# Kernel tuning notes

Measured on AMD Instinct MI355X. Metric: run time of the kernel, lower is better.

The kernel has to match this reference:

```python
import jax, jax.numpy as jnp
import numpy as np

B, C, D, T = 8, 512, 256, 2048
EPS = 1e-5


def setup_inputs() -> dict:
    key = jax.random.key(0)
    ks = jax.random.split(key, 9)
    s_c = 1.0 / np.sqrt(C)
    s_d = 1.0 / np.sqrt(D)
    return {
        "inpt": jax.random.normal(ks[0], (B, C, T), dtype=jnp.float32),
        "theta_w": jax.random.uniform(ks[1], (D, C), jnp.float32, -s_c, s_c),
        "theta_b": jax.random.uniform(ks[2], (D,), jnp.float32, -s_c, s_c),
        "phi_w": jax.random.uniform(ks[3], (D, C), jnp.float32, -s_c, s_c),
        "phi_b": jax.random.uniform(ks[4], (D,), jnp.float32, -s_c, s_c),
        "g_w": jax.random.uniform(ks[5], (D, C), jnp.float32, -s_c, s_c),
        "g_b": jax.random.uniform(ks[6], (D,), jnp.float32, -s_c, s_c),
        "ht_w": jax.random.uniform(ks[7], (C, D), jnp.float32, -s_d, s_d),
        "ht_b": jax.random.uniform(ks[8], (C,), jnp.float32, -s_d, s_d),
        "bn_gamma": jnp.ones((C,), dtype=jnp.float32),
        "bn_beta": jnp.zeros((C,), dtype=jnp.float32),
    }


def reference(inpt, theta_w, theta_b, phi_w, phi_b, g_w, g_b, ht_w, ht_b, bn_gamma, bn_beta):
    # 1x1 convs are just channel-mixing matmuls: (B,C,T) -> (B,D,T)
    theta = jnp.einsum('dc,bct->bdt', theta_w, inpt) + theta_b[None, :, None]
    phi = jnp.einsum('dc,bct->bdt', phi_w, inpt) + phi_b[None, :, None]
    g = jnp.einsum('dc,bct->bdt', g_w, inpt) + g_b[None, :, None]
    # w[b,t,s] = sum_d theta[b,d,t] * phi[b,d,s]; softmax over s (phi time)
    w = jnp.einsum('bdt,bds->bts', theta, phi)
    w = jax.nn.softmax(w, axis=-1)
    # torch.matmul(g, w): out[b,d,s] = sum_t g[b,d,t] * w[b,t,s]
    attn = jnp.einsum('bdt,bts->bds', g, w)
    # ht 1x1 conv back to C channels
    h = jnp.einsum('cd,bdt->bct', ht_w, attn) + ht_b[None, :, None]
    # BatchNorm1d in training mode: batch stats over (B, T) per channel
    mean = jnp.mean(h, axis=(0, 2), keepdims=True)
    var = jnp.var(h, axis=(0, 2), keepdims=True)  # biased variance
    h_norm = (h - mean) * jax.lax.rsqrt(var + EPS)
    bn = bn_gamma[None, :, None] * h_norm + bn_beta[None, :, None]
    return inpt + bn
```

## Files before the change

kernel.cpp:

```cpp
#include <hip/hip_runtime.h>
#include <hip/hip_bf16.h>
#include <math.h>

#define Bx 8
#define Cx 512
#define Dx 256
#define Tx 2048
#define EPSx 1e-5f

typedef _Float16 h16;
typedef __attribute__((ext_vector_type(8))) _Float16 h16x8;
typedef __attribute__((ext_vector_type(8))) short s16x8;
typedef __attribute__((ext_vector_type(4))) float f32x4;

typedef __attribute__((address_space(3))) unsigned int lds_u32;
typedef __attribute__((address_space(1))) const unsigned int glb_u32;

__device__ __forceinline__ void cp16(void* ldsp, const void* g) {
    __builtin_amdgcn_global_load_lds((glb_u32*)g, (lds_u32*)ldsp, 16, 0, 0);
}

template<int MODE, bool BF>
__global__ __launch_bounds__(256, 4)
void gemm_mf(const h16* __restrict__ A, long aBatch, int lda,
             const h16* __restrict__ B, long bBatch, int ldb,
             void* __restrict__ C, long cBatch, int ldc,
             float* __restrict__ Cp, float* __restrict__ Z,
             int M, int N, int K,
             const float* __restrict__ biasM, const float* __restrict__ biasN) {
    __shared__ h16 As[128 * 64];
    __shared__ h16 Bs[128 * 64];
    const int tid  = threadIdx.x;
    const int lane = tid & 63, wid = tid >> 6;
    const int wm = (wid & 1) * 64, wn = (wid >> 1) * 64;
    const int lm = lane & 15, quad = lane >> 4;
    const int m0 = blockIdx.y * 128, n0 = blockIdx.x * 128;
    const int b = blockIdx.z;
    const h16* Ab = A + (size_t)b * aBatch + (size_t)m0 * lda;
    const h16* Bb = B + (size_t)b * bBatch + (size_t)n0 * ldb;

    const int srow  = tid >> 3;
    const int sclog = (tid & 7) ^ (srow & 7);
    char* ldsA = (char*)As + (tid & ~63) * 16;
    char* ldsB = (char*)Bs + (tid & ~63) * 16;

    f32x4 acc[4][4] = {};

    for (int k0 = 0; k0 < K; k0 += 64) {
        __syncthreads();
#pragma unroll
        for (int i = 0; i < 4; i++) {
            int r = srow + 32 * i;
            cp16(ldsA + i * 4096, Ab + (size_t)r * lda + k0 + sclog * 8);
        }
#pragma unroll
        for (int i = 0; i < 4; i++) {
            int r = srow + 32 * i;
            cp16(ldsB + i * 4096, Bb + (size_t)r * ldb + k0 + sclog * 8);
        }
        __syncthreads();
#pragma unroll
        for (int ks = 0; ks < 2; ks++) {
            s16x8 af[4], bf4[4];
#pragma unroll
            for (int i = 0; i < 4; i++) {
                int row = wm + 16 * i + lm;
                int st = (ks * 4 + quad) ^ (lm & 7);
                af[i] = *(const s16x8*)(As + row * 64 + st * 8);
            }
#pragma unroll
            for (int j = 0; j < 4; j++) {
                int row = wn + 16 * j + lm;
                int st = (ks * 4 + quad) ^ (lm & 7);
                bf4[j] = *(const s16x8*)(Bs + row * 64 + st * 8);
            }
#pragma unroll
            for (int i = 0; i < 4; i++)
#pragma unroll
                for (int j = 0; j < 4; j++) {
                    if constexpr (BF)
                        acc[i][j] = __builtin_amdgcn_mfma_f32_16x16x32_bf16(
                            af[i], bf4[j], acc[i][j], 0, 0, 0);
                    else
                        acc[i][j] = __builtin_amdgcn_mfma_f32_16x16x32_f16(
                            __builtin_bit_cast(h16x8, af[i]),
                            __builtin_bit_cast(h16x8, bf4[j]), acc[i][j], 0, 0, 0);
                }
        }
    }

    if constexpr (MODE == 0) {
        h16* Cb = (h16*)C + (size_t)b * cBatch;
#pragma unroll
        for (int i = 0; i < 4; i++)
#pragma unroll
            for (int j = 0; j < 4; j++) {
                int row = m0 + wm + 16 * i + quad * 4;
                int col = n0 + wn + 16 * j + lm;
                float bN = biasN ? biasN[col] : 0.0f;
#pragma unroll
                for (int r = 0; r < 4; r++) {
                    float v = acc[i][j][r] + bN;
                    if (biasM) v += biasM[row + r];
                    Cb[(size_t)(row + r) * ldc + col] = (h16)v;
                }
            }
    } else if constexpr (MODE == 1) {
        __hip_bfloat16* Cb = (__hip_bfloat16*)C + (size_t)b * cBatch;
#pragma unroll
        for (int j = 0; j < 4; j++) {
            int col = n0 + wn + 16 * j + lm;
            float iz = 1.0f / Z[(size_t)b * N + col];
#pragma unroll
            for (int i = 0; i < 4; i++) {
                int row = m0 + wm + 16 * i + quad * 4;
#pragma unroll
                for (int r = 0; r < 4; r++)
                    Cb[(size_t)(row + r) * ldc + col] =
                        __float2bfloat16(acc[i][j][r] * iz);
            }
        }
    } else if constexpr (MODE == 2) {
        __syncthreads();
        float* Zl = (float*)As;
        if (tid < 128) Zl[tid] = 0.0f;
        __syncthreads();
        __hip_bfloat16* Cb = (__hip_bfloat16*)C + (size_t)b * cBatch;
#pragma unroll
        for (int j = 0; j < 4; j++) {
            int cl = wn + 16 * j + lm;
            int col = n0 + cl;
            float zp = 0.0f;
#pragma unroll
            for (int i = 0; i < 4; i++) {
                int row = m0 + wm + 16 * i + quad * 4;
#pragma unroll
                for (int r = 0; r < 4; r++) {
                    float e = __expf(acc[i][j][r]);
                    zp += e;
                    Cb[(size_t)(row + r) * ldc + col] = __float2bfloat16(e);
                }
            }
            atomicAdd(&Zl[cl], zp);
        }
        __syncthreads();
        if (tid < 128) atomicAdd(&Z[(size_t)b * N + n0 + tid], Zl[tid]);
    } else {
        __syncthreads();
        float* Sl = (float*)As;
        float* Sq = Sl + 128;
        if (tid < 256) Sl[tid] = 0.0f;
        __syncthreads();
        h16* Cb = (h16*)C + (size_t)b * cBatch;
#pragma unroll
        for (int j = 0; j < 4; j++) {
            int cl = wn + 16 * j + lm;
            int col = n0 + cl;
            float bN = biasN[col];
            float s = 0.0f, q = 0.0f;
#pragma unroll
            for (int i = 0; i < 4; i++) {
                int row = m0 + wm + 16 * i + quad * 4;
#pragma unroll
                for (int r = 0; r < 4; r++) {
                    float v = acc[i][j][r] + bN;
                    s += v;
                    q = fmaf(v, v, q);
                    Cb[(size_t)(row + r) * ldc + col] = (h16)v;
                }
            }
            atomicAdd(&Sl[cl], s);
            atomicAdd(&Sq[cl], q);
        }
        __syncthreads();
        if (tid < 128) {
            atomicAdd(&Cp[n0 + tid], Sl[tid]);
            atomicAdd(&Z[n0 + tid], Sq[tid]);
        }
    }
}

__global__ __launch_bounds__(256)
void conv_x(const float* __restrict__ inpt, h16* __restrict__ xT) {
    __shared__ float lds[64][68];
    const int b = blockIdx.z;
    const int t0 = blockIdx.x * 64, c0 = blockIdx.y * 64;
    const int tid = threadIdx.x, q = tid >> 4, k = tid & 15;
    const float* ib = inpt + (size_t)b * Cx * Tx;
#pragma unroll
    for (int i = 0; i < 4; i++) {
        int c = q + 16 * i;
        float4 v = *(const float4*)(ib + (size_t)(c0 + c) * Tx + t0 + 4 * k);
        *(float4*)&lds[c][4 * k] = v;
    }
    __syncthreads();
    h16* xb = xT + (size_t)b * Tx * Cx;
#pragma unroll
    for (int i = 0; i < 4; i++) {
        int t = q + 16 * i;
        h16 o[4];
#pragma unroll
        for (int j = 0; j < 4; j++) o[j] = (h16)lds[4 * k + j][t];
        *(uint2*)(xb + (size_t)(t0 + t) * Cx + c0 + 4 * k) = *(uint2*)o;
    }
}

__global__ __launch_bounds__(256)
void conv_w(const float* __restrict__ w0, const float* __restrict__ w1,
            const float* __restrict__ w2, const float* __restrict__ w3,
            const float* __restrict__ tb, const float* __restrict__ pb,
            const float* __restrict__ gb,
            h16* __restrict__ dst, float* __restrict__ bias3,
            float* __restrict__ Z, float* __restrict__ psum,
            float* __restrict__ pssq) {
    int bx = blockIdx.x;
    int tid = threadIdx.x;
    if (bx == 577) {
        psum[tid] = 0.0f; psum[tid + 256] = 0.0f;
        pssq[tid] = 0.0f; pssq[tid + 256] = 0.0f;
        return;
    }
    if (bx >= 513) { Z[(bx - 513) * 256 + tid] = 0.0f; return; }
    if (bx == 512) {
        bias3[tid] = tb[tid];
        bias3[tid + 256] = pb[tid];
        bias3[tid + 512] = gb[tid];
        return;
    }
    int idx4 = bx * 256 + tid;
    int arr = idx4 >> 15, local4 = idx4 & 32767;
    const float* srcs[4] = {w0, w1, w2, w3};
    float4 v = ((const float4*)srcs[arr])[local4];
    h16 o[4] = {(h16)v.x, (h16)v.y, (h16)v.z, (h16)v.w};
    *(uint2*)(dst + (size_t)arr * 131072 + (size_t)local4 * 4) = *(uint2*)o;
}

__global__ __launch_bounds__(256)
void bn_final(const float* __restrict__ psum, const float* __restrict__ pssq,
              float* __restrict__ mean, float* __restrict__ rsig) {
    int c = blockIdx.x * 256 + threadIdx.x;
    const float invN = 1.0f / (float)(Bx * Tx);
    float mu = psum[c] * invN;
    float var = pssq[c] * invN - mu * mu;
    mean[c] = mu;
    rsig[c] = rsqrtf(var + EPSx);
}

__global__ __launch_bounds__(256)
void bn_apply_T(const float* __restrict__ inpt, const h16* __restrict__ hT,
                const float* __restrict__ mean, const float* __restrict__ rsig,
                const float* __restrict__ gamma, const float* __restrict__ beta,
                float* __restrict__ out) {
    __shared__ float lds[64][68];
    const int b = blockIdx.z, t0 = blockIdx.x * 64, c0 = blockIdx.y * 64;
    const int tid = threadIdx.x, q = tid >> 4, k = tid & 15;
    const h16* hb = hT + (size_t)b * Tx * Cx;
#pragma unroll
    for (int i = 0; i < 4; i++) {
        int t = q + 16 * i;
        uint2 raw = *(const uint2*)(hb + (size_t)(t0 + t) * Cx + c0 + 4 * k);
        const h16* hp = (const h16*)&raw;
        float4 v = make_float4((float)hp[0], (float)hp[1], (float)hp[2], (float)hp[3]);
        *(float4*)&lds[t][4 * k] = v;
    }
    __syncthreads();
    const float* ib = inpt + (size_t)b * Cx * Tx;
    float* ob = out + (size_t)b * Cx * Tx;
#pragma unroll
    for (int i = 0; i < 4; i++) {
        int c = q + 16 * i;
        int cg = c0 + c;
        float mu = mean[cg], rv = rsig[cg], ga = gamma[cg], be = beta[cg];
        float4 x = *(const float4*)(ib + (size_t)cg * Tx + t0 + 4 * k);
        float4 o;
        o.x = x.x + ga * (lds[4 * k + 0][c] - mu) * rv + be;
        o.y = x.y + ga * (lds[4 * k + 1][c] - mu) * rv + be;
        o.z = x.z + ga * (lds[4 * k + 2][c] - mu) * rv + be;
        o.w = x.w + ga * (lds[4 * k + 3][c] - mu) * rv + be;
        *(float4*)(ob + (size_t)cg * Tx + t0 + 4 * k) = o;
    }
}

extern "C" void kernel_launch(void* const* d_in, const int* in_sizes, int n_in,
                              void* d_out, int out_size, void* d_ws, size_t ws_size,
                              hipStream_t stream) {
    const float* inpt    = (const float*)d_in[0];
    const float* theta_w = (const float*)d_in[1];
    const float* theta_b = (const float*)d_in[2];
    const float* phi_w   = (const float*)d_in[3];
    const float* phi_b   = (const float*)d_in[4];
    const float* g_w     = (const float*)d_in[5];
    const float* g_b     = (const float*)d_in[6];
    const float* ht_w    = (const float*)d_in[7];
    const float* ht_b    = (const float*)d_in[8];
    const float* gamma   = (const float*)d_in[9];
    const float* beta    = (const float*)d_in[10];

    char* ws = (char*)d_ws;
    h16*   xT    = (h16*)(ws + 0);
    h16*   w4    = (h16*)(ws + 16777216);
    h16*   wHt   = w4 + 393216;
    float* bias3 = (float*)(ws + 17825792);
    float* Z     = (float*)(ws + 17828864);
    float* psum  = (float*)(ws + 17894400);
    float* pssq  = (float*)(ws + 17896448);
    float* mu    = (float*)(ws + 17898496);
    float* rs    = (float*)(ws + 17900544);
    h16*   thpg  = (h16*)(ws + 17902592);
    h16*   gh    = (h16*)(ws + 43068416);
    h16*   LT    = (h16*)(ws + 59845632);
    h16*   hT    = xT;

    const long sX  = (long)Tx * Cx;
    const long sTP = (long)Tx * 768;
    const long sGH = (long)Cx * Tx;
    const long sW  = (long)Tx * Tx;

    dim3 blk(256);
    conv_x<<<dim3(Tx / 64, Cx / 64, Bx), blk, 0, stream>>>(inpt, xT);
    conv_w<<<578, blk, 0, stream>>>(theta_w, phi_w, g_w, ht_w,
                                    theta_b, phi_b, g_b,
                                    w4, bias3, Z, psum, pssq);
    gemm_mf<0, false><<<dim3(6, 16, Bx), blk, 0, stream>>>(
        xT, sX, Cx, w4, 0, Cx, thpg, sTP, 768, nullptr, nullptr,
        Tx, 768, Cx, nullptr, bias3);
    gemm_mf<2, false><<<dim3(16, 16, Bx), blk, 0, stream>>>(
        thpg + 256, sTP, 768, thpg, sTP, 768, LT, sW, Tx, nullptr, Z,
        Tx, Tx, Dx, nullptr, nullptr);
    gemm_mf<1, false><<<dim3(16, 4, Bx), blk, 0, stream>>>(
        wHt, 0, Dx, thpg + 512, sTP, 768, gh, sGH, Tx, nullptr, Z,
        Cx, Tx, Dx, nullptr, nullptr);
    gemm_mf<3, true><<<dim3(4, 16, Bx), blk, 0, stream>>>(
        LT, sW, Tx, gh, sGH, Tx, hT, sX, Cx, psum, pssq,
        Tx, Cx, Tx, nullptr, ht_b);
    bn_final<<<2, blk, 0, stream>>>(psum, pssq, mu, rs);
    bn_apply_T<<<dim3(Tx / 64, Cx / 64, Bx), blk, 0, stream>>>(
        inpt, hT, mu, rs, gamma, beta, (float*)d_out);
}
```

Baseline: 236.6 us.

## Widen K tile for attention-apply GEMM, remap its blocks, fold BN finalize

The GEMM kernel now takes its K-tile depth as a template parameter, and the large K=2048 attention-apply GEMM uses a 128-deep tile to halve its barrier and load-issue rounds. That GEMM also switches to a 1D grid with the batch index in the low bits, so consecutive blocks cover different batches, which changes how concurrent blocks share cache. The separate bn_final kernel is removed, and mean/rsqrt are computed inline in bn_apply_T, saving one launch. The larger tile doubles LDS per block (64 KB) and may lower occupancy. The swizzle only XORs 3 bits while the tile now has 16 chunks per row, which may raise LDS bank conflicts.

```diff
diff --git a/kernel.cpp b/kernel.cpp
--- a/kernel.cpp
+++ b/kernel.cpp
@@ -20,7 +20,7 @@
     __builtin_amdgcn_global_load_lds((glb_u32*)g, (lds_u32*)ldsp, 16, 0, 0);
 }
 
-template<int MODE, bool BF>
+template<int MODE, bool BF, int BK>
 __global__ __launch_bounds__(256, 4)
 void gemm_mf(const h16* __restrict__ A, long aBatch, int lda,
              const h16* __restrict__ B, long bBatch, int ldb,
@@ -28,51 +28,62 @@
              float* __restrict__ Cp, float* __restrict__ Z,
              int M, int N, int K,
              const float* __restrict__ biasM, const float* __restrict__ biasN) {
-    __shared__ h16 As[128 * 64];
-    __shared__ h16 Bs[128 * 64];
+    __shared__ h16 As[128 * BK];
+    __shared__ h16 Bs[128 * BK];
     const int tid  = threadIdx.x;
     const int lane = tid & 63, wid = tid >> 6;
     const int wm = (wid & 1) * 64, wn = (wid >> 1) * 64;
     const int lm = lane & 15, quad = lane >> 4;
-    const int m0 = blockIdx.y * 128, n0 = blockIdx.x * 128;
-    const int b = blockIdx.z;
+    int m0, n0, b;
+    if constexpr (MODE == 3) {
+        int id = blockIdx.x;
+        b = id & 7;
+        int rr = id >> 3;
+        m0 = (rr & 15) << 7;
+        n0 = (rr >> 4) << 7;
+    } else {
+        m0 = blockIdx.y * 128; n0 = blockIdx.x * 128; b = blockIdx.z;
+    }
     const h16* Ab = A + (size_t)b * aBatch + (size_t)m0 * lda;
     const h16* Bb = B + (size_t)b * bBatch + (size_t)n0 * ldb;
 
-    const int srow  = tid >> 3;
-    const int sclog = (tid & 7) ^ (srow & 7);
+    constexpr int CH  = BK / 8;
+    constexpr int RPR = 2048 / BK;
+    constexpr int RND = BK / 16;
+    const int srow  = tid / CH;
+    const int sclog = (tid & (CH - 1)) ^ (srow & 7);
     char* ldsA = (char*)As + (tid & ~63) * 16;
     char* ldsB = (char*)Bs + (tid & ~63) * 16;
 
     f32x4 acc[4][4] = {};
 
-    for (int k0 = 0; k0 < K; k0 += 64) {
-        __syncthreads();
-#pragma unroll
-        for (int i = 0; i < 4; i++) {
-            int r = srow + 32 * i;
+    for (int k0 = 0; k0 < K; k0 += BK) {
+        __syncthreads();
+#pragma unroll
+        for (int i = 0; i < RND; i++) {
+            int r = srow + RPR * i;
             cp16(ldsA + i * 4096, Ab + (size_t)r * lda + k0 + sclog * 8);
         }
 #pragma unroll
-        for (int i = 0; i < 4; i++) {
-            int r = srow + 32 * i;
+        for (int i = 0; i < RND; i++) {
+            int r = srow + RPR * i;
             cp16(ldsB + i * 4096, Bb + (size_t)r * ldb + k0 + sclog * 8);
         }
         __syncthreads();
 #pragma unroll
-        for (int ks = 0; ks < 2; ks++) {
+        for (int ks = 0; ks < BK / 32; ks++) {
             s16x8 af[4], bf4[4];
 #pragma unroll
             for (int i = 0; i < 4; i++) {
                 int row = wm + 16 * i + lm;
                 int st = (ks * 4 + quad) ^ (lm & 7);
-                af[i] = *(const s16x8*)(As + row * 64 + st * 8);
+                af[i] = *(const s16x8*)(As + row * BK + st * 8);
             }
 #pragma unroll
             for (int j = 0; j < 4; j++) {
                 int row = wn + 16 * j + lm;
                 int st = (ks * 4 + quad) ^ (lm & 7);
-                bf4[j] = *(const s16x8*)(Bs + row * 64 + st * 8);
+                bf4[j] = *(const s16x8*)(Bs + row * BK + st * 8);
             }
 #pragma unroll
             for (int i = 0; i < 4; i++)
@@ -236,19 +247,8 @@
 }
 
 __global__ __launch_bounds__(256)
-void bn_final(const float* __restrict__ psum, const float* __restrict__ pssq,
-              float* __restrict__ mean, float* __restrict__ rsig) {
-    int c = blockIdx.x * 256 + threadIdx.x;
-    const float invN = 1.0f / (float)(Bx * Tx);
-    float mu = psum[c] * invN;
-    float var = pssq[c] * invN - mu * mu;
-    mean[c] = mu;
-    rsig[c] = rsqrtf(var + EPSx);
-}
-
-__global__ __launch_bounds__(256)
 void bn_apply_T(const float* __restrict__ inpt, const h16* __restrict__ hT,
-                const float* __restrict__ mean, const float* __restrict__ rsig,
+                const float* __restrict__ psum, const float* __restrict__ pssq,
                 const float* __restrict__ gamma, const float* __restrict__ beta,
                 float* __restrict__ out) {
     __shared__ float lds[64][68];
@@ -266,11 +266,15 @@
     __syncthreads();
     const float* ib = inpt + (size_t)b * Cx * Tx;
     float* ob = out + (size_t)b * Cx * Tx;
+    const float invN = 1.0f / (float)(Bx * Tx);
 #pragma unroll
     for (int i = 0; i < 4; i++) {
         int c = q + 16 * i;
         int cg = c0 + c;
-        float mu = mean[cg], rv = rsig[cg], ga = gamma[cg], be = beta[cg];
+        float mu = psum[cg] * invN;
+        float var = pssq[cg] * invN - mu * mu;
+        float rv = rsqrtf(var + EPSx);
+        float ga = gamma[cg], be = beta[cg];
         float4 x = *(const float4*)(ib + (size_t)cg * Tx + t0 + 4 * k);
         float4 o;
         o.x = x.x + ga * (lds[4 * k + 0][c] - mu) * rv + be;
@@ -304,8 +308,6 @@
     float* Z     = (float*)(ws + 17828864);
     float* psum  = (float*)(ws + 17894400);
     float* pssq  = (float*)(ws + 17896448);
-    float* mu    = (float*)(ws + 17898496);
-    float* rs    = (float*)(ws + 17900544);
     h16*   thpg  = (h16*)(ws + 17902592);
     h16*   gh    = (h16*)(ws + 43068416);
     h16*   LT    = (h16*)(ws + 59845632);
@@ -321,19 +323,18 @@
     conv_w<<<578, blk, 0, stream>>>(theta_w, phi_w, g_w, ht_w,
                                     theta_b, phi_b, g_b,
                                     w4, bias3, Z, psum, pssq);
-    gemm_mf<0, false><<<dim3(6, 16, Bx), blk, 0, stream>>>(
+    gemm_mf<0, false, 64><<<dim3(6, 16, Bx), blk, 0, stream>>>(
         xT, sX, Cx, w4, 0, Cx, thpg, sTP, 768, nullptr, nullptr,
         Tx, 768, Cx, nullptr, bias3);
-    gemm_mf<2, false><<<dim3(16, 16, Bx), blk, 0, stream>>>(
+    gemm_mf<2, false, 64><<<dim3(16, 16, Bx), blk, 0, stream>>>(
         thpg + 256, sTP, 768, thpg, sTP, 768, LT, sW, Tx, nullptr, Z,
         Tx, Tx, Dx, nullptr, nullptr);
-    gemm_mf<1, false><<<dim3(16, 4, Bx), blk, 0, stream>>>(
+    gemm_mf<1, false, 64><<<dim3(16, 4, Bx), blk, 0, stream>>>(
         wHt, 0, Dx, thpg + 512, sTP, 768, gh, sGH, Tx, nullptr, Z,
         Cx, Tx, Dx, nullptr, nullptr);
-    gemm_mf<3, true><<<dim3(4, 16, Bx), blk, 0, stream>>>(
+    gemm_mf<3, true, 128><<<dim3(512), blk, 0, stream>>>(
         LT, sW, Tx, gh, sGH, Tx, hT, sX, Cx, psum, pssq,
         Tx, Cx, Tx, nullptr, ht_b);
-    bn_final<<<2, blk, 0, stream>>>(psum, pssq, mu, rs);
     bn_apply_T<<<dim3(Tx / 64, Cx / 64, Bx), blk, 0, stream>>>(
-        inpt, hT, mu, rs, gamma, beta, (float*)d_out);
-}
+        inpt, hT, psum, pssq, gamma, beta, (float*)d_out);
+}
```

New measurement: 229.1 us. 3.2% less time.
